# Optimization experiments

Hardware: AMD Instinct MI355X
Metric: run time of the kernel (lower is better)

The kernel has to match this reference:

```python
import jax, jax.numpy as jnp
import numpy as np

N_HEADS = 8
D_EMBED = 512
D_HEAD = D_EMBED // N_HEADS  # used only for the scale factor, as in the source


def setup_inputs() -> dict:
    key = jax.random.key(0)
    k1, k2, k3, k4, k5 = jax.random.split(key, 5)
    B, S, D = 4, 4096, D_EMBED
    s = 1.0 / np.sqrt(D)
    return {
        "x": jax.random.normal(k1, (B, S, D), dtype=jnp.float32),
        "w_in": jax.random.normal(k2, (3 * D, D), dtype=jnp.float32) * s,
        "b_in": jax.random.normal(k3, (3 * D,), dtype=jnp.float32) * 0.01,
        "w_out": jax.random.normal(k4, (D, D), dtype=jnp.float32) * s,
        "b_out": jax.random.normal(k5, (D,), dtype=jnp.float32) * 0.01,
    }


def reference(x, w_in, b_in, w_out, b_out):
    # in_proj: torch Linear y = x @ W.T + b ; chunk into q,k,v along last dim
    qkv = jnp.einsum("bsd,ed->bse", x, w_in) + b_in  # [B,S,3D]
    q, k, v = jnp.split(qkv, 3, axis=-1)  # each [B,S,D]
    # NOTE: source never splits into heads; attention over full d_embed,
    # but scaled by sqrt(d_head) = sqrt(d_embed / n_heads).
    scores = jnp.einsum("bqd,bkd->bqk", q, k) / np.sqrt(D_HEAD)  # [B,S,S]
    weight = jax.nn.softmax(scores, axis=-1)
    out = jnp.einsum("bqk,bkd->bqd", weight, v)  # [B,S,D]
    out = jnp.einsum("bsd,ed->bse", out, w_out) + b_out
    return out
```

## Files before the change

kernel.cpp:

```cpp
#include <hip/hip_runtime.h>

typedef __bf16 bf16x8 __attribute__((ext_vector_type(8)));
typedef float f32x4 __attribute__((ext_vector_type(4)));

#define MFMA16(a, b, c) __builtin_amdgcn_mfma_f32_16x16x32_bf16(a, b, c, 0, 0, 0)
#define LOG2E 1.44269504088896340736f

__device__ __forceinline__ unsigned short f2bf(float f) {
  union { float f; unsigned u; } v; v.f = f;
  return (unsigned short)((v.u + 0x7fffu + ((v.u >> 16) & 1u)) >> 16);
}
__device__ __forceinline__ bf16x8 ld_frag(const unsigned short* p) {
  return *(const bf16x8*)p;
}
__device__ __forceinline__ void gld_lds16(const unsigned short* g, unsigned short* l) {
  __builtin_amdgcn_global_load_lds(
      (const __attribute__((address_space(1))) unsigned int*)(const void*)g,
      (__attribute__((address_space(3))) unsigned int*)(void*)l, 16, 0, 0);
}

__global__ void cvt_f2bf(const float* __restrict__ in,
                         unsigned short* __restrict__ out, int n4) {
  int i = blockIdx.x * blockDim.x + threadIdx.x;
  if (i < n4) {
    float4 v = ((const float4*)in)[i];
    ushort4 o;
    o.x = f2bf(v.x); o.y = f2bf(v.y); o.z = f2bf(v.z); o.w = f2bf(v.w);
    ((ushort4*)out)[i] = o;
  }
}

__global__ void gemm_bt(const unsigned short* __restrict__ A,
                        const unsigned short* __restrict__ B,
                        const float* __restrict__ bias,
                        float* __restrict__ outf,
                        unsigned short* __restrict__ qbuf,
                        unsigned short* __restrict__ kbuf,
                        unsigned short* __restrict__ vtbuf,
                        int M, int N, int K, int mode) {
  __shared__ alignas(16) unsigned short As[128 * 32];
  __shared__ alignas(16) unsigned short Bs[128 * 32];
  const int n0 = blockIdx.x * 128, m0 = blockIdx.y * 128;
  const int tid = threadIdx.x;
  const int l = tid & 63, w = tid >> 6;
  const int quad = l >> 4, c = l & 15;
  const int wm = (w >> 1) * 64, wn = (w & 1) * 64;

  f32x4 acc[4][4] = {};
  const int kiters = K >> 5;
  for (int kt = 0; kt < kiters; ++kt) {
    __syncthreads();
    const int kk = kt * 32 + (l & 3) * 8;
    const int row = l >> 2;
#pragma unroll
    for (int i = 0; i < 2; ++i) {
      const int rbase = i * 64 + w * 16;
      gld_lds16(&A[(size_t)(m0 + rbase + row) * K + kk], &As[rbase * 32]);
      gld_lds16(&B[(size_t)(n0 + rbase + row) * K + kk], &Bs[rbase * 32]);
    }
    __syncthreads();
    bf16x8 af[4], bfr[4];
#pragma unroll
    for (int t = 0; t < 4; ++t) {
      af[t] = ld_frag(&As[(wm + t * 16 + c) * 32 + quad * 8]);
      bfr[t] = ld_frag(&Bs[(wn + t * 16 + c) * 32 + quad * 8]);
    }
#pragma unroll
    for (int mt = 0; mt < 4; ++mt)
#pragma unroll
      for (int nt = 0; nt < 4; ++nt)
        acc[mt][nt] = MFMA16(af[mt], bfr[nt], acc[mt][nt]);
  }

#pragma unroll
  for (int nt = 0; nt < 4; ++nt) {
    const int n = n0 + wn + nt * 16 + c;
    const float bsum = bias[n];
#pragma unroll
    for (int mt = 0; mt < 4; ++mt) {
      const int mbase = m0 + wm + mt * 16 + quad * 4;
      if (mode == 0) {
#pragma unroll
        for (int r = 0; r < 4; ++r)
          outf[(size_t)(mbase + r) * N + n] = acc[mt][nt][r] + bsum;
      } else if (n < 1024) {
        unsigned short* dst = (n < 512) ? qbuf : kbuf;
        const int nn = n & 511;
#pragma unroll
        for (int r = 0; r < 4; ++r)
          dst[(size_t)(mbase + r) * 512 + nn] = f2bf(acc[mt][nt][r] + bsum);
      } else {
        const int d = n - 1024;
        const int bb = mbase >> 12, s = mbase & 4095;
        ushort4 pk;
        pk.x = f2bf(acc[mt][nt][0] + bsum);
        pk.y = f2bf(acc[mt][nt][1] + bsum);
        pk.z = f2bf(acc[mt][nt][2] + bsum);
        pk.w = f2bf(acc[mt][nt][3] + bsum);
        *(ushort4*)&vtbuf[((size_t)bb * 512 + d) * 4096 + s] = pk;
      }
    }
  }
}

#define KROW 520
#define PROW 40

__global__ __launch_bounds__(256, 2) void attn_kernel(
    const unsigned short* __restrict__ Q, const unsigned short* __restrict__ Kb,
    const unsigned short* __restrict__ Vt, unsigned short* __restrict__ part0,
    unsigned short* __restrict__ part1, float2* __restrict__ mlbuf) {
  __shared__ alignas(16) unsigned short k_lds[32 * KROW];
  __shared__ alignas(16) unsigned short v_lds[512 * 32];
  __shared__ alignas(16) unsigned short p_lds[64 * PROW];
  __shared__ float alpha_s[64];
  __shared__ int flag_s[4];

  const int bid = blockIdx.x;
  const int xcd = bid & 7;
  const int b = xcd >> 1;
  const int half = (bid >> 3) & 1;
  const int qt = (bid >> 4) | ((xcd & 1) << 5);
  const int s0 = qt * 64;
  const int kvbase = half * 2048;
  const int tid = threadIdx.x;
  const int l = tid & 63, w = tid >> 6;
  const int quad = l >> 4, c = l & 15;
  const size_t boff = (size_t)b * 4096 * 512;

  bf16x8 qf[16];
  {
    const unsigned short* qrow = Q + boff + (size_t)(s0 + w * 16 + c) * 512;
#pragma unroll
    for (int ks = 0; ks < 16; ++ks) qf[ks] = ld_frag(&qrow[ks * 32 + quad * 8]);
  }

  f32x4 o[8][4] = {};
  float m_run = -1e30f, l_run = 0.f;

  const unsigned short* Kbase = Kb + boff;
  const unsigned short* Vbase = Vt + (size_t)b * 512 * 4096;

  auto stage_k = [&](int kv0) {
#pragma unroll
    for (int i = 0; i < 8; ++i) {
      const int row = i * 4 + w;
      gld_lds16(&Kbase[(size_t)(kv0 + row) * 512 + l * 8], &k_lds[row * KROW]);
    }
  };
  auto stage_v = [&](int kv0) {
#pragma unroll
    for (int i = 0; i < 8; ++i) {
      const int dbase = (i * 4 + w) * 16;
      const int d = dbase + (l >> 2);
      const int jl = (l & 3) ^ ((d >> 1) & 3);
      gld_lds16(&Vbase[(size_t)d * 4096 + kv0 + jl * 8], &v_lds[dbase * 32]);
    }
  };

  stage_k(kvbase);
  stage_v(kvbase);

  const int jp8 = (quad ^ ((c >> 1) & 3)) * 8;

  for (int it = 0; it < 64; ++it) {
    __syncthreads();

    f32x4 sa[2][2] = {};
#pragma unroll
    for (int ks = 0; ks < 16; ++ks) {
      const unsigned short* kr = &k_lds[c * KROW + ks * 32 + quad * 8];
      bf16x8 kf0 = ld_frag(kr);
      bf16x8 kf1 = ld_frag(kr + 16 * KROW);
      sa[0][ks & 1] = MFMA16(kf0, qf[ks], sa[0][ks & 1]);
      sa[1][ks & 1] = MFMA16(kf1, qf[ks], sa[1][ks & 1]);
    }
    const f32x4 s0v = sa[0][0] + sa[0][1];
    const f32x4 s1v = sa[1][0] + sa[1][1];

    const float C1 = 0.125f * LOG2E;
    float m8 = fmaxf(fmaxf(fmaxf(s0v[0], s0v[1]), fmaxf(s0v[2], s0v[3])),
                     fmaxf(fmaxf(s1v[0], s1v[1]), fmaxf(s1v[2], s1v[3])));
    m8 = fmaxf(m8, __shfl_xor(m8, 16));
    m8 = fmaxf(m8, __shfl_xor(m8, 32));

    const bool need = __any(m8 - m_run > 8.0f);
    float alpha = 1.0f;
    if (need) {
      const float mn = fmaxf(m_run, m8);
      alpha = exp2f((m_run - mn) * C1);
      m_run = mn;
      l_run *= alpha;
    }

    float p0[4], p1[4], s8 = 0.f;
#pragma unroll
    for (int r = 0; r < 4; ++r) {
      p0[r] = exp2f((s0v[r] - m_run) * C1);
      p1[r] = exp2f((s1v[r] - m_run) * C1);
      s8 += p0[r] + p1[r];
    }
    unsigned short* prow = &p_lds[(w * 16 + c) * PROW];
    ushort4 pk0, pk1;
    pk0.x = f2bf(p0[0]); pk0.y = f2bf(p0[1]); pk0.z = f2bf(p0[2]); pk0.w = f2bf(p0[3]);
    pk1.x = f2bf(p1[0]); pk1.y = f2bf(p1[1]); pk1.z = f2bf(p1[2]); pk1.w = f2bf(p1[3]);
    *(ushort4*)&prow[quad * 4] = pk0;
    *(ushort4*)&prow[16 + quad * 4] = pk1;

    s8 += __shfl_xor(s8, 16);
    s8 += __shfl_xor(s8, 32);
    l_run += s8;

    if (quad == 0) alpha_s[w * 16 + c] = alpha;
    if (l == 0) flag_s[w] = need ? 1 : 0;

    __syncthreads();

    if (it + 1 < 64) stage_k(kvbase + (it + 1) * 32);

    const int f0 = flag_s[0], f1 = flag_s[1], f2 = flag_s[2], f3 = flag_s[3];
    if (f0) {
      const float a = alpha_s[c];
#pragma unroll
      for (int t = 0; t < 8; ++t) o[t][0] *= a;
    }
    if (f1) {
      const float a = alpha_s[16 + c];
#pragma unroll
      for (int t = 0; t < 8; ++t) o[t][1] *= a;
    }
    if (f2) {
      const float a = alpha_s[32 + c];
#pragma unroll
      for (int t = 0; t < 8; ++t) o[t][2] *= a;
    }
    if (f3) {
      const float a = alpha_s[48 + c];
#pragma unroll
      for (int t = 0; t < 8; ++t) o[t][3] *= a;
    }

    const bf16x8 pf0 = ld_frag(&p_lds[(size_t)c * PROW + quad * 8]);
    const bf16x8 pf1 = ld_frag(&p_lds[(size_t)(16 + c) * PROW + quad * 8]);
    const bf16x8 pf2 = ld_frag(&p_lds[(size_t)(32 + c) * PROW + quad * 8]);
    const bf16x8 pf3 = ld_frag(&p_lds[(size_t)(48 + c) * PROW + quad * 8]);
#pragma unroll
    for (int t = 0; t < 8; ++t) {
      const bf16x8 vf = ld_frag(&v_lds[(w * 128 + t * 16 + c) * 32 + jp8]);
      o[t][0] = MFMA16(vf, pf0, o[t][0]);
      o[t][1] = MFMA16(vf, pf1, o[t][1]);
      o[t][2] = MFMA16(vf, pf2, o[t][2]);
      o[t][3] = MFMA16(vf, pf3, o[t][3]);
    }

    __syncthreads();
    if (it + 1 < 64) stage_v(kvbase + (it + 1) * 32);
  }

  if (quad == 0) {
    alpha_s[w * 16 + c] = l_run;
    float2 ml; ml.x = m_run; ml.y = l_run;
    mlbuf[(size_t)half * 16384 + b * 4096 + s0 + w * 16 + c] = ml;
  }
  __syncthreads();
  const float linv0 = 1.0f / alpha_s[c];
  const float linv1 = 1.0f / alpha_s[16 + c];
  const float linv2 = 1.0f / alpha_s[32 + c];
  const float linv3 = 1.0f / alpha_s[48 + c];

  unsigned short* part = half ? part1 : part0;
  unsigned short* obase = part + boff + (size_t)s0 * 512 + w * 128 + quad * 4;
#pragma unroll
  for (int t = 0; t < 8; ++t) {
    const float li[4] = {linv0, linv1, linv2, linv3};
#pragma unroll
    for (int j = 0; j < 4; ++j) {
      ushort4 pk;
      pk.x = f2bf(o[t][j][0] * li[j]);
      pk.y = f2bf(o[t][j][1] * li[j]);
      pk.z = f2bf(o[t][j][2] * li[j]);
      pk.w = f2bf(o[t][j][3] * li[j]);
      *(ushort4*)&obase[(size_t)(j * 16 + c) * 512 + t * 16] = pk;
    }
  }
}

__global__ void merge_halves(const unsigned short* __restrict__ p1,
                             const float2* __restrict__ mlbuf,
                             unsigned short* __restrict__ p0out) {
  const int i = blockIdx.x * blockDim.x + threadIdx.x;
  const int row = i >> 6;
  const float2 a = mlbuf[row];
  const float2 bb = mlbuf[16384 + row];
  const float C1 = 0.125f * LOG2E;
  const float M = fmaxf(a.x, bb.x);
  float w0 = a.y * exp2f((a.x - M) * C1);
  float w1 = bb.y * exp2f((bb.x - M) * C1);
  const float inv = 1.0f / (w0 + w1);
  w0 *= inv; w1 *= inv;
  bf16x8 v0 = *(const bf16x8*)(p0out + (size_t)i * 8);
  bf16x8 v1 = *(const bf16x8*)(p1 + (size_t)i * 8);
  ushort4 o0, o1;
  o0.x = f2bf(w0 * (float)v0[0] + w1 * (float)v1[0]);
  o0.y = f2bf(w0 * (float)v0[1] + w1 * (float)v1[1]);
  o0.z = f2bf(w0 * (float)v0[2] + w1 * (float)v1[2]);
  o0.w = f2bf(w0 * (float)v0[3] + w1 * (float)v1[3]);
  o1.x = f2bf(w0 * (float)v0[4] + w1 * (float)v1[4]);
  o1.y = f2bf(w0 * (float)v0[5] + w1 * (float)v1[5]);
  o1.z = f2bf(w0 * (float)v0[6] + w1 * (float)v1[6]);
  o1.w = f2bf(w0 * (float)v0[7] + w1 * (float)v1[7]);
  *(ushort4*)(p0out + (size_t)i * 8) = o0;
  *(ushort4*)(p0out + (size_t)i * 8 + 4) = o1;
}

extern "C" void kernel_launch(void* const* d_in, const int* in_sizes, int n_in,
                              void* d_out, int out_size, void* d_ws, size_t ws_size,
                              hipStream_t stream) {
  const float* x = (const float*)d_in[0];
  const float* w_in = (const float*)d_in[1];
  const float* b_in = (const float*)d_in[2];
  const float* w_out = (const float*)d_in[3];
  const float* b_out = (const float*)d_in[4];
  float* out = (float*)d_out;

  const size_t MTOT = (size_t)4 * 4096 * 512;
  unsigned short* q = (unsigned short*)d_ws;
  unsigned short* k = q + MTOT;
  unsigned short* vt = k + MTOT;
  unsigned short* xbf = vt + MTOT;
  unsigned short* part1 = xbf + MTOT;
  unsigned short* w_in_bf = part1 + MTOT;
  unsigned short* w_out_bf = w_in_bf + 1536 * 512;
  float2* mlbuf = (float2*)(w_out_bf + 512 * 512);

  cvt_f2bf<<<dim3((int)(MTOT / 4 / 256)), 256, 0, stream>>>(x, xbf,
                                                            (int)(MTOT / 4));
  cvt_f2bf<<<dim3(768), 256, 0, stream>>>(w_in, w_in_bf, 1536 * 512 / 4);
  cvt_f2bf<<<dim3(256), 256, 0, stream>>>(w_out, w_out_bf, 512 * 512 / 4);

  gemm_bt<<<dim3(12, 128), 256, 0, stream>>>(xbf, w_in_bf, b_in, nullptr, q, k,
                                             vt, 16384, 1536, 512, 1);
  attn_kernel<<<dim3(512), 256, 0, stream>>>(q, k, vt, xbf, part1, mlbuf);
  merge_halves<<<dim3(4096), 256, 0, stream>>>(part1, mlbuf, xbf);
  gemm_bt<<<dim3(4, 128), 256, 0, stream>>>(xbf, w_out_bf, b_out, out, nullptr,
                                            nullptr, nullptr, 16384, 512, 512,
                                            0);
}
```

Baseline: 413.8 us.

## Double-buffer K in LDS and load V fragments directly from global

Double-buffers the K tile in LDS so the next tile's async global-to-LDS load is issued at the top of each iteration and overlaps the QK^T MFMAs. V staging through LDS is removed: each wave reads its V^T fragments straight from global memory (L2) inside the PV loop. One barrier per iteration is dropped, manual waitcnt and sched_barrier placement is added, and s_setprio raises wave priority around the MFMA loops. The direct V loads put global latency on the PV critical path with no prefetch, and uncoalesced 16-byte row reads per lane could cost more than the LDS staging they replace.

```diff
diff --git a/kernel.cpp b/kernel.cpp
--- a/kernel.cpp
+++ b/kernel.cpp
@@ -105,13 +105,13 @@
 
 #define KROW 520
 #define PROW 40
+#define KBUF (32 * KROW)
 
 __global__ __launch_bounds__(256, 2) void attn_kernel(
     const unsigned short* __restrict__ Q, const unsigned short* __restrict__ Kb,
     const unsigned short* __restrict__ Vt, unsigned short* __restrict__ part0,
     unsigned short* __restrict__ part1, float2* __restrict__ mlbuf) {
-  __shared__ alignas(16) unsigned short k_lds[32 * KROW];
-  __shared__ alignas(16) unsigned short v_lds[512 * 32];
+  __shared__ alignas(16) unsigned short k_lds[2 * KBUF];
   __shared__ alignas(16) unsigned short p_lds[64 * PROW];
   __shared__ float alpha_s[64];
   __shared__ int flag_s[4];
@@ -128,6 +128,19 @@
   const int quad = l >> 4, c = l & 15;
   const size_t boff = (size_t)b * 4096 * 512;
 
+  const unsigned short* Kbase = Kb + boff;
+
+  auto stage_k = [&](int kv0, int bufbase) {
+#pragma unroll
+    for (int i = 0; i < 8; ++i) {
+      const int row = i * 4 + w;
+      gld_lds16(&Kbase[(size_t)(kv0 + row) * 512 + l * 8],
+                &k_lds[bufbase + row * KROW]);
+    }
+  };
+
+  stage_k(kvbase, 0);
+
   bf16x8 qf[16];
   {
     const unsigned short* qrow = Q + boff + (size_t)(s0 + w * 16 + c) * 512;
@@ -138,43 +151,29 @@
   f32x4 o[8][4] = {};
   float m_run = -1e30f, l_run = 0.f;
 
-  const unsigned short* Kbase = Kb + boff;
-  const unsigned short* Vbase = Vt + (size_t)b * 512 * 4096;
-
-  auto stage_k = [&](int kv0) {
-#pragma unroll
-    for (int i = 0; i < 8; ++i) {
-      const int row = i * 4 + w;
-      gld_lds16(&Kbase[(size_t)(kv0 + row) * 512 + l * 8], &k_lds[row * KROW]);
-    }
-  };
-  auto stage_v = [&](int kv0) {
-#pragma unroll
-    for (int i = 0; i < 8; ++i) {
-      const int dbase = (i * 4 + w) * 16;
-      const int d = dbase + (l >> 2);
-      const int jl = (l & 3) ^ ((d >> 1) & 3);
-      gld_lds16(&Vbase[(size_t)d * 4096 + kv0 + jl * 8], &v_lds[dbase * 32]);
-    }
-  };
-
-  stage_k(kvbase);
-  stage_v(kvbase);
-
-  const int jp8 = (quad ^ ((c >> 1) & 3)) * 8;
+  const unsigned short* vrow = Vt + (size_t)b * 512 * 4096 +
+                               (size_t)(w * 128 + c) * 4096 + kvbase + quad * 8;
 
   for (int it = 0; it < 64; ++it) {
-    __syncthreads();
+    const int cb = (it & 1) * KBUF;
+
+    asm volatile("s_waitcnt vmcnt(0)" ::: "memory");
+    __builtin_amdgcn_s_barrier();
+    __builtin_amdgcn_sched_barrier(0);
+
+    if (it + 1 < 64) stage_k(kvbase + (it + 1) * 32, KBUF - cb);
 
     f32x4 sa[2][2] = {};
+    __builtin_amdgcn_s_setprio(1);
 #pragma unroll
     for (int ks = 0; ks < 16; ++ks) {
-      const unsigned short* kr = &k_lds[c * KROW + ks * 32 + quad * 8];
+      const unsigned short* kr = &k_lds[cb + c * KROW + ks * 32 + quad * 8];
       bf16x8 kf0 = ld_frag(kr);
       bf16x8 kf1 = ld_frag(kr + 16 * KROW);
       sa[0][ks & 1] = MFMA16(kf0, qf[ks], sa[0][ks & 1]);
       sa[1][ks & 1] = MFMA16(kf1, qf[ks], sa[1][ks & 1]);
     }
+    __builtin_amdgcn_s_setprio(0);
     const f32x4 s0v = sa[0][0] + sa[0][1];
     const f32x4 s1v = sa[1][0] + sa[1][1];
 
@@ -214,9 +213,10 @@
     if (quad == 0) alpha_s[w * 16 + c] = alpha;
     if (l == 0) flag_s[w] = need ? 1 : 0;
 
-    __syncthreads();
-
-    if (it + 1 < 64) stage_k(kvbase + (it + 1) * 32);
+    asm volatile("s_waitcnt lgkmcnt(0)" ::: "memory");
+    __builtin_amdgcn_sched_barrier(0);
+    __builtin_amdgcn_s_barrier();
+    __builtin_amdgcn_sched_barrier(0);
 
     const int f0 = flag_s[0], f1 = flag_s[1], f2 = flag_s[2], f3 = flag_s[3];
     if (f0) {
@@ -244,19 +244,20 @@
     const bf16x8 pf1 = ld_frag(&p_lds[(size_t)(16 + c) * PROW + quad * 8]);
     const bf16x8 pf2 = ld_frag(&p_lds[(size_t)(32 + c) * PROW + quad * 8]);
     const bf16x8 pf3 = ld_frag(&p_lds[(size_t)(48 + c) * PROW + quad * 8]);
+    const unsigned short* vi = vrow + it * 32;
+    __builtin_amdgcn_s_setprio(1);
 #pragma unroll
     for (int t = 0; t < 8; ++t) {
-      const bf16x8 vf = ld_frag(&v_lds[(w * 128 + t * 16 + c) * 32 + jp8]);
+      const bf16x8 vf = ld_frag(vi + (size_t)t * 16 * 4096);
       o[t][0] = MFMA16(vf, pf0, o[t][0]);
       o[t][1] = MFMA16(vf, pf1, o[t][1]);
       o[t][2] = MFMA16(vf, pf2, o[t][2]);
       o[t][3] = MFMA16(vf, pf3, o[t][3]);
     }
-
-    __syncthreads();
-    if (it + 1 < 64) stage_v(kvbase + (it + 1) * 32);
-  }
-
+    __builtin_amdgcn_s_setprio(0);
+  }
+
+  __syncthreads();
   if (quad == 0) {
     alpha_s[w * 16 + c] = l_run;
     float2 ml; ml.x = m_run; ml.y = l_run;
```

Result: slower. 456.3 us (+10.3%).

## Software-pipeline QK softmax with V staging using double-buffered P tiles

Applied to the files above, without the earlier changes.

The attention loop is reordered so that the QK^T plus softmax for the next KV tile runs right after the next V tile's global-to-LDS load is issued, instead of waiting behind a barrier. The P tile in LDS is double-buffered by iteration parity, and the __syncthreads calls are replaced with explicit waitcnt and s_barrier pairs; vmcnt(8) lets only the K loads complete before QK starts. MFMA sections are wrapped in s_setprio to favour matrix issue. The aim is to hide V load latency behind QK compute, at the cost of more LDS for P and more fragile hand-placed synchronisation.

```diff
diff --git a/kernel.cpp b/kernel.cpp
--- a/kernel.cpp
+++ b/kernel.cpp
@@ -105,6 +105,7 @@
 
 #define KROW 520
 #define PROW 40
+#define PBUF (64 * PROW)
 
 __global__ __launch_bounds__(256, 2) void attn_kernel(
     const unsigned short* __restrict__ Q, const unsigned short* __restrict__ Kb,
@@ -112,7 +113,7 @@
     unsigned short* __restrict__ part1, float2* __restrict__ mlbuf) {
   __shared__ alignas(16) unsigned short k_lds[32 * KROW];
   __shared__ alignas(16) unsigned short v_lds[512 * 32];
-  __shared__ alignas(16) unsigned short p_lds[64 * PROW];
+  __shared__ alignas(16) unsigned short p_lds[2 * PBUF];
   __shared__ float alpha_s[64];
   __shared__ int flag_s[4];
 
@@ -128,16 +129,6 @@
   const int quad = l >> 4, c = l & 15;
   const size_t boff = (size_t)b * 4096 * 512;
 
-  bf16x8 qf[16];
-  {
-    const unsigned short* qrow = Q + boff + (size_t)(s0 + w * 16 + c) * 512;
-#pragma unroll
-    for (int ks = 0; ks < 16; ++ks) qf[ks] = ld_frag(&qrow[ks * 32 + quad * 8]);
-  }
-
-  f32x4 o[8][4] = {};
-  float m_run = -1e30f, l_run = 0.f;
-
   const unsigned short* Kbase = Kb + boff;
   const unsigned short* Vbase = Vt + (size_t)b * 512 * 4096;
 
@@ -161,12 +152,21 @@
   stage_k(kvbase);
   stage_v(kvbase);
 
-  const int jp8 = (quad ^ ((c >> 1) & 3)) * 8;
-
-  for (int it = 0; it < 64; ++it) {
-    __syncthreads();
-
+  bf16x8 qf[16];
+  {
+    const unsigned short* qrow = Q + boff + (size_t)(s0 + w * 16 + c) * 512;
+#pragma unroll
+    for (int ks = 0; ks < 16; ++ks) qf[ks] = ld_frag(&qrow[ks * 32 + quad * 8]);
+  }
+
+  f32x4 o[8][4] = {};
+  float m_run = -1e30f, l_run = 0.f;
+
+  const float C1 = 0.125f * LOG2E;
+
+  auto qk_softmax = [&](int i) {
     f32x4 sa[2][2] = {};
+    __builtin_amdgcn_s_setprio(1);
 #pragma unroll
     for (int ks = 0; ks < 16; ++ks) {
       const unsigned short* kr = &k_lds[c * KROW + ks * 32 + quad * 8];
@@ -175,10 +175,10 @@
       sa[0][ks & 1] = MFMA16(kf0, qf[ks], sa[0][ks & 1]);
       sa[1][ks & 1] = MFMA16(kf1, qf[ks], sa[1][ks & 1]);
     }
+    __builtin_amdgcn_s_setprio(0);
     const f32x4 s0v = sa[0][0] + sa[0][1];
     const f32x4 s1v = sa[1][0] + sa[1][1];
 
-    const float C1 = 0.125f * LOG2E;
     float m8 = fmaxf(fmaxf(fmaxf(s0v[0], s0v[1]), fmaxf(s0v[2], s0v[3])),
                      fmaxf(fmaxf(s1v[0], s1v[1]), fmaxf(s1v[2], s1v[3])));
     m8 = fmaxf(m8, __shfl_xor(m8, 16));
@@ -200,7 +200,7 @@
       p1[r] = exp2f((s1v[r] - m_run) * C1);
       s8 += p0[r] + p1[r];
     }
-    unsigned short* prow = &p_lds[(w * 16 + c) * PROW];
+    unsigned short* prow = &p_lds[(i & 1) * PBUF + (w * 16 + c) * PROW];
     ushort4 pk0, pk1;
     pk0.x = f2bf(p0[0]); pk0.y = f2bf(p0[1]); pk0.z = f2bf(p0[2]); pk0.w = f2bf(p0[3]);
     pk1.x = f2bf(p1[0]); pk1.y = f2bf(p1[1]); pk1.z = f2bf(p1[2]); pk1.w = f2bf(p1[3]);
@@ -213,8 +213,21 @@
 
     if (quad == 0) alpha_s[w * 16 + c] = alpha;
     if (l == 0) flag_s[w] = need ? 1 : 0;
-
-    __syncthreads();
+  };
+
+  const int jp8 = (quad ^ ((c >> 1) & 3)) * 8;
+
+  asm volatile("s_waitcnt vmcnt(0)" ::: "memory");
+  __builtin_amdgcn_sched_barrier(0);
+  __builtin_amdgcn_s_barrier();
+  __builtin_amdgcn_sched_barrier(0);
+  qk_softmax(0);
+
+  for (int it = 0; it < 64; ++it) {
+    asm volatile("s_waitcnt vmcnt(0) lgkmcnt(0)" ::: "memory");
+    __builtin_amdgcn_sched_barrier(0);
+    __builtin_amdgcn_s_barrier();
+    __builtin_amdgcn_sched_barrier(0);
 
     if (it + 1 < 64) stage_k(kvbase + (it + 1) * 32);
 
@@ -240,10 +253,12 @@
       for (int t = 0; t < 8; ++t) o[t][3] *= a;
     }
 
-    const bf16x8 pf0 = ld_frag(&p_lds[(size_t)c * PROW + quad * 8]);
-    const bf16x8 pf1 = ld_frag(&p_lds[(size_t)(16 + c) * PROW + quad * 8]);
-    const bf16x8 pf2 = ld_frag(&p_lds[(size_t)(32 + c) * PROW + quad * 8]);
-    const bf16x8 pf3 = ld_frag(&p_lds[(size_t)(48 + c) * PROW + quad * 8]);
+    const unsigned short* pb = &p_lds[(it & 1) * PBUF];
+    const bf16x8 pf0 = ld_frag(&pb[(size_t)c * PROW + quad * 8]);
+    const bf16x8 pf1 = ld_frag(&pb[(size_t)(16 + c) * PROW + quad * 8]);
+    const bf16x8 pf2 = ld_frag(&pb[(size_t)(32 + c) * PROW + quad * 8]);
+    const bf16x8 pf3 = ld_frag(&pb[(size_t)(48 + c) * PROW + quad * 8]);
+    __builtin_amdgcn_s_setprio(1);
 #pragma unroll
     for (int t = 0; t < 8; ++t) {
       const bf16x8 vf = ld_frag(&v_lds[(w * 128 + t * 16 + c) * 32 + jp8]);
@@ -252,9 +267,21 @@
       o[t][2] = MFMA16(vf, pf2, o[t][2]);
       o[t][3] = MFMA16(vf, pf3, o[t][3]);
     }
-
-    __syncthreads();
-    if (it + 1 < 64) stage_v(kvbase + (it + 1) * 32);
+    __builtin_amdgcn_s_setprio(0);
+
+    asm volatile("s_waitcnt lgkmcnt(0)" ::: "memory");
+    __builtin_amdgcn_sched_barrier(0);
+    __builtin_amdgcn_s_barrier();
+    __builtin_amdgcn_sched_barrier(0);
+
+    if (it + 1 < 64) {
+      stage_v(kvbase + (it + 1) * 32);
+      asm volatile("s_waitcnt vmcnt(8)" ::: "memory");
+      __builtin_amdgcn_sched_barrier(0);
+      __builtin_amdgcn_s_barrier();
+      __builtin_amdgcn_sched_barrier(0);
+      qk_softmax(it + 1);
+    }
   }
 
   if (quad == 0) {
```

Measured after the change: 413.0 us. No clear change (-0.2%).
